# Optimization experiments

Hardware: AMD Instinct MI355X
Metric: run time of the kernel (lower is better)

Reference implementation:

```python
import jax, jax.numpy as jnp
import numpy as np
import math

B, T, H = 16, 4096, 768
D = 64      # attention_head_size
M = 256     # number of random features


def setup_inputs() -> dict:
    key = jax.random.key(0)
    ks = jax.random.split(key, 8)
    s = 1.0 / math.sqrt(H)
    x = jax.random.normal(ks[0], (B, T, H), dtype=jnp.float32)
    Wq = jax.random.uniform(ks[1], (H, D), jnp.float32, -s, s)
    bq = jax.random.uniform(ks[2], (D,), jnp.float32, -s, s)
    Wk = jax.random.uniform(ks[3], (H, D), jnp.float32, -s, s)
    bk = jax.random.uniform(ks[4], (D,), jnp.float32, -s, s)
    Wv = jax.random.uniform(ks[5], (H, D), jnp.float32, -s, s)
    bv = jax.random.uniform(ks[6], (D,), jnp.float32, -s, s)
    w = jax.random.normal(ks[7], (M, D), dtype=jnp.float32)  # frozen random features
    return {"x": x, "Wq": Wq, "bq": bq, "Wk": Wk, "bk": bk, "Wv": Wv, "bv": bv, "w": w}


def _prm_exp(z, w):
    # z: [B,T,D], w: [M,D] -> [B,T,M]
    xd = 0.5 * jnp.sum(z * z, axis=-1, keepdims=True)          # [B,T,1]
    wtx = jnp.einsum('bti,mi->btm', z, w)                      # [B,T,M]
    return jnp.exp(wtx - xd) / math.sqrt(w.shape[0])


def reference(x, Wq, bq, Wk, bk, Wv, bv, w):
    q = x @ Wq + bq                                            # [B,T,D]
    k = x @ Wk + bk
    v = x @ Wv + bv
    qp = _prm_exp(q, w)                                        # [B,T,M]
    kp = _prm_exp(k, w)                                        # [B,T,M]
    Dn = jnp.einsum('bti,bi->bt', qp, kp.sum(axis=1))[:, :, None]   # [B,T,1]
    kptv = jnp.einsum('bin,bim->bnm', v, kp)                   # [B,D,M]
    attn_out = jnp.einsum('bti,bni->btn', qp, kptv) / Dn       # [B,T,D]
    return attn_out, kptv
```

## Files before the change

kernel.cpp:

```cpp
#include <hip/hip_runtime.h>
#include <math.h>

#define BB 16
#define TT 4096
#define HH 768
#define DD 64
#define MM 256
#define BT (BB*TT)
#define TSPLIT 16

__device__ __forceinline__ void fma4(float& acc, float4 a, float4 b){
    acc = __builtin_fmaf(a.x, b.x, acc);
    acc = __builtin_fmaf(a.y, b.y, acc);
    acc = __builtin_fmaf(a.z, b.z, acc);
    acc = __builtin_fmaf(a.w, b.w, acc);
}

__global__ __launch_bounds__(256) void qkv_kernel(
    const float* __restrict__ x,
    const float* __restrict__ Wq, const float* __restrict__ bq,
    const float* __restrict__ Wk, const float* __restrict__ bk,
    const float* __restrict__ Wv, const float* __restrict__ bv,
    float* __restrict__ q, float* __restrict__ k, float* __restrict__ v)
{
    __shared__ float xs[64][36];
    __shared__ float ws[32][196];
    const int tid = threadIdx.x;
    const int row0 = blockIdx.x * 64;
    const int tr = tid >> 4, tc = tid & 15;

    float4 acc[4][3];
    #pragma unroll
    for (int r = 0; r < 4; r++)
        #pragma unroll
        for (int c = 0; c < 3; c++) acc[r][c] = make_float4(0.f,0.f,0.f,0.f);

    for (int kc = 0; kc < HH; kc += 32){
        __syncthreads();
        #pragma unroll
        for (int i = 0; i < 2; i++){
            int l = tid + i*256;
            int r = l >> 3, j4 = (l & 7) << 2;
            *(float4*)&xs[r][j4] = *(const float4*)&x[(size_t)(row0+r)*HH + kc + j4];
        }
        #pragma unroll
        for (int i = 0; i < 2; i++){
            int l = tid + i*256;
            int kk = l >> 4, c4 = (l & 15) << 2;
            *(float4*)&ws[kk][c4]       = *(const float4*)&Wq[(size_t)(kc+kk)*DD + c4];
            *(float4*)&ws[kk][64 + c4]  = *(const float4*)&Wk[(size_t)(kc+kk)*DD + c4];
            *(float4*)&ws[kk][128 + c4] = *(const float4*)&Wv[(size_t)(kc+kk)*DD + c4];
        }
        __syncthreads();
        #pragma unroll
        for (int kk = 0; kk < 32; kk++){
            float xv[4];
            float4 wv[3];
            #pragma unroll
            for (int r = 0; r < 4; r++) xv[r] = xs[tr*4+r][kk];
            #pragma unroll
            for (int c = 0; c < 3; c++) wv[c] = *(float4*)&ws[kk][tc*12 + c*4];
            #pragma unroll
            for (int r = 0; r < 4; r++)
                #pragma unroll
                for (int c = 0; c < 3; c++){
                    acc[r][c].x = __builtin_fmaf(xv[r], wv[c].x, acc[r][c].x);
                    acc[r][c].y = __builtin_fmaf(xv[r], wv[c].y, acc[r][c].y);
                    acc[r][c].z = __builtin_fmaf(xv[r], wv[c].z, acc[r][c].z);
                    acc[r][c].w = __builtin_fmaf(xv[r], wv[c].w, acc[r][c].w);
                }
        }
    }
    #pragma unroll
    for (int c = 0; c < 3; c++){
        int col = tc*12 + c*4;
        int sel = col >> 6;
        int d = col & 63;
        const float* bias = (sel==0) ? bq : (sel==1) ? bk : bv;
        float* dst = (sel==0) ? q : (sel==1) ? k : v;
        float4 b4 = *(const float4*)&bias[d];
        #pragma unroll
        for (int r = 0; r < 4; r++){
            size_t grow = (size_t)(row0 + tr*4 + r);
            float4 o;
            o.x = acc[r][c].x + b4.x;
            o.y = acc[r][c].y + b4.y;
            o.z = acc[r][c].z + b4.z;
            o.w = acc[r][c].w + b4.w;
            *(float4*)&dst[grow*DD + d] = o;
        }
    }
}

__global__ __launch_bounds__(256) void kp_kernel(
    const float* __restrict__ k, const float* __restrict__ w,
    float* __restrict__ kp, float* __restrict__ ksum)
{
    __shared__ float ks_[64][68];
    __shared__ float ws_[64][68];
    __shared__ float xd_s[64];
    __shared__ float ksum_s[256];
    const int tid = threadIdx.x;
    const int row0 = blockIdx.x * 64;
    const int b = row0 >> 12;
    const int tr = tid >> 4, tc = tid & 15;

    #pragma unroll
    for (int i = 0; i < 4; i++){
        int l = tid + i*256;
        int r = l >> 4, c4 = (l & 15) << 2;
        *(float4*)&ks_[r][c4] = *(const float4*)&k[(size_t)(row0+r)*DD + c4];
    }
    ksum_s[tid] = 0.f;
    __syncthreads();
    {
        int rowx = tid >> 2, sub = tid & 3;
        float s = 0.f;
        #pragma unroll
        for (int j = 0; j < 4; j++){
            float4 kv = *(float4*)&ks_[rowx][sub*16 + j*4];
            s += kv.x*kv.x + kv.y*kv.y + kv.z*kv.z + kv.w*kv.w;
        }
        s += __shfl_xor(s, 1);
        s += __shfl_xor(s, 2);
        if (sub == 0) xd_s[rowx] = 0.5f * s;
    }

    for (int mc = 0; mc < 4; mc++){
        __syncthreads();
        #pragma unroll
        for (int i = 0; i < 4; i++){
            int l = tid + i*256;
            int r = l >> 4, c4 = (l & 15) << 2;
            *(float4*)&ws_[r][c4] = *(const float4*)&w[(size_t)(mc*64 + r)*DD + c4];
        }
        __syncthreads();
        float acc[4][4];
        #pragma unroll
        for (int r = 0; r < 4; r++)
            #pragma unroll
            for (int c = 0; c < 4; c++) acc[r][c] = 0.f;
        #pragma unroll
        for (int d4 = 0; d4 < 16; d4++){
            float4 qv[4], wv[4];
            #pragma unroll
            for (int r = 0; r < 4; r++) qv[r] = *(float4*)&ks_[tr*4+r][d4*4];
            #pragma unroll
            for (int c = 0; c < 4; c++) wv[c] = *(float4*)&ws_[tc + 16*c][d4*4];
            #pragma unroll
            for (int r = 0; r < 4; r++)
                #pragma unroll
                for (int c = 0; c < 4; c++) fma4(acc[r][c], qv[r], wv[c]);
        }
        float colsum[4] = {0.f, 0.f, 0.f, 0.f};
        #pragma unroll
        for (int r = 0; r < 4; r++){
            float xd = xd_s[tr*4+r];
            #pragma unroll
            for (int c = 0; c < 4; c++){
                float val = expf(acc[r][c] - xd) * 0.0625f;
                colsum[c] += val;
                kp[(size_t)(row0 + tr*4 + r)*MM + mc*64 + tc + 16*c] = val;
            }
        }
        #pragma unroll
        for (int c = 0; c < 4; c++)
            atomicAdd(&ksum_s[mc*64 + tc + 16*c], colsum[c]);
    }
    __syncthreads();
    unsafeAtomicAdd(&ksum[b*MM + tid], ksum_s[tid]);
}

__global__ __launch_bounds__(256) void kptv_kernel(
    const float* __restrict__ v, const float* __restrict__ kp,
    float* __restrict__ out_kptv)
{
    __shared__ float vs[32][68];
    __shared__ float kps[32][68];
    const int tid = threadIdx.x;
    const int b  = blockIdx.z;
    const int mc = blockIdx.y;
    const int t0 = blockIdx.x * (TT/TSPLIT);
    const int tn = tid >> 4, tm = tid & 15;

    float acc[4][4];
    #pragma unroll
    for (int r = 0; r < 4; r++)
        #pragma unroll
        for (int c = 0; c < 4; c++) acc[r][c] = 0.f;

    for (int tt = 0; tt < TT/TSPLIT; tt += 32){
        __syncthreads();
        #pragma unroll
        for (int i = 0; i < 2; i++){
            int l = tid + i*256;
            int r = l >> 4, c4 = (l & 15) << 2;
            *(float4*)&vs[r][c4]  = *(const float4*)&v [(size_t)(b*TT + t0 + tt + r)*DD + c4];
            *(float4*)&kps[r][c4] = *(const float4*)&kp[(size_t)(b*TT + t0 + tt + r)*MM + mc*64 + c4];
        }
        __syncthreads();
        #pragma unroll
        for (int t = 0; t < 32; t++){
            float vv[4], kv[4];
            *(float4*)vv = *(float4*)&vs[t][tn*4];
            *(float4*)kv = *(float4*)&kps[t][tm*4];
            #pragma unroll
            for (int r = 0; r < 4; r++)
                #pragma unroll
                for (int c = 0; c < 4; c++)
                    acc[r][c] = __builtin_fmaf(vv[r], kv[c], acc[r][c]);
        }
    }
    #pragma unroll
    for (int r = 0; r < 4; r++)
        #pragma unroll
        for (int c = 0; c < 4; c++)
            unsafeAtomicAdd(&out_kptv[(size_t)b*DD*MM + (size_t)(tn*4+r)*MM + mc*64 + tm*4 + c],
                            acc[r][c]);
}

__global__ __launch_bounds__(256) void attn_kernel(
    const float* __restrict__ q, const float* __restrict__ w,
    const float* __restrict__ kptv, const float* __restrict__ ksum,
    float* __restrict__ out)
{
    __shared__ float qs[64][68];
    __shared__ float wqp[64][68];
    __shared__ float kvs[64][68];
    __shared__ float ksum_s[256];
    __shared__ float xd_s[64];
    const int tid = threadIdx.x;
    const int row0 = blockIdx.x * 64;
    const int b = row0 >> 12;
    const int tr = tid >> 4, tc = tid & 15;

    #pragma unroll
    for (int i = 0; i < 4; i++){
        int l = tid + i*256;
        int r = l >> 4, c4 = (l & 15) << 2;
        *(float4*)&qs[r][c4] = *(const float4*)&q[(size_t)(row0 + r)*DD + c4];
    }
    ksum_s[tid] = ksum[b*MM + tid];
    __syncthreads();
    {
        int rowx = tid >> 2, sub = tid & 3;
        float s = 0.f;
        #pragma unroll
        for (int j = 0; j < 4; j++){
            float4 qv = *(float4*)&qs[rowx][sub*16 + j*4];
            s += qv.x*qv.x + qv.y*qv.y + qv.z*qv.z + qv.w*qv.w;
        }
        s += __shfl_xor(s, 1);
        s += __shfl_xor(s, 2);
        if (sub == 0) xd_s[rowx] = 0.5f * s;
    }

    float acc2[4][4];
    float dn[4];
    #pragma unroll
    for (int r = 0; r < 4; r++){
        dn[r] = 0.f;
        #pragma unroll
        for (int c = 0; c < 4; c++) acc2[r][c] = 0.f;
    }

    for (int mc = 0; mc < 4; mc++){
        __syncthreads();
        #pragma unroll
        for (int i = 0; i < 4; i++){
            int l = tid + i*256;
            int r = l >> 4, c4 = (l & 15) << 2;
            *(float4*)&wqp[r][c4] = *(const float4*)&w[(size_t)(mc*64 + r)*DD + c4];
            *(float4*)&kvs[r][c4] = *(const float4*)&kptv[(size_t)b*DD*MM + r*MM + mc*64 + c4];
        }
        __syncthreads();
        float acc1[4][4];
        #pragma unroll
        for (int r = 0; r < 4; r++)
            #pragma unroll
            for (int c = 0; c < 4; c++) acc1[r][c] = 0.f;
        #pragma unroll
        for (int d4 = 0; d4 < 16; d4++){
            float4 qv[4], wv[4];
            #pragma unroll
            for (int r = 0; r < 4; r++) qv[r] = *(float4*)&qs[tr*4+r][d4*4];
            #pragma unroll
            for (int c = 0; c < 4; c++) wv[c] = *(float4*)&wqp[tc + 16*c][d4*4];
            #pragma unroll
            for (int r = 0; r < 4; r++)
                #pragma unroll
                for (int c = 0; c < 4; c++) fma4(acc1[r][c], qv[r], wv[c]);
        }
        float qp_[4][4];
        #pragma unroll
        for (int r = 0; r < 4; r++){
            float xd = xd_s[tr*4+r];
            #pragma unroll
            for (int c = 0; c < 4; c++){
                float val = expf(acc1[r][c] - xd) * 0.0625f;
                qp_[r][c] = val;
                dn[r] = __builtin_fmaf(val, ksum_s[mc*64 + tc + 16*c], dn[r]);
            }
        }
        __syncthreads();
        #pragma unroll
        for (int r = 0; r < 4; r++)
            #pragma unroll
            for (int c = 0; c < 4; c++)
                wqp[tr*4+r][tc + 16*c] = qp_[r][c];
        __syncthreads();
        #pragma unroll
        for (int m4 = 0; m4 < 16; m4++){
            float4 qv[4], kv[4];
            #pragma unroll
            for (int r = 0; r < 4; r++) qv[r] = *(float4*)&wqp[tr*4+r][m4*4];
            #pragma unroll
            for (int c = 0; c < 4; c++) kv[c] = *(float4*)&kvs[tc + 16*c][m4*4];
            #pragma unroll
            for (int r = 0; r < 4; r++)
                #pragma unroll
                for (int c = 0; c < 4; c++) fma4(acc2[r][c], qv[r], kv[c]);
        }
    }
    #pragma unroll
    for (int r = 0; r < 4; r++){
        dn[r] += __shfl_xor(dn[r], 1);
        dn[r] += __shfl_xor(dn[r], 2);
        dn[r] += __shfl_xor(dn[r], 4);
        dn[r] += __shfl_xor(dn[r], 8);
    }
    #pragma unroll
    for (int r = 0; r < 4; r++){
        float inv = 1.0f / dn[r];
        #pragma unroll
        for (int c = 0; c < 4; c++)
            out[(size_t)(row0 + tr*4 + r)*DD + tc + 16*c] = acc2[r][c] * inv;
    }
}

extern "C" void kernel_launch(void* const* d_in, const int* in_sizes, int n_in,
                              void* d_out, int out_size, void* d_ws, size_t ws_size,
                              hipStream_t stream) {
    const float* x  = (const float*)d_in[0];
    const float* Wq = (const float*)d_in[1];
    const float* bq = (const float*)d_in[2];
    const float* Wk = (const float*)d_in[3];
    const float* bk = (const float*)d_in[4];
    const float* Wv = (const float*)d_in[5];
    const float* bv = (const float*)d_in[6];
    const float* w  = (const float*)d_in[7];

    float* out_attn = (float*)d_out;
    float* out_kptv = out_attn + (size_t)BB*TT*DD;

    float* q    = (float*)d_ws;
    float* k    = q + (size_t)BT*DD;
    float* v    = k + (size_t)BT*DD;
    float* kp   = v + (size_t)BT*DD;
    float* ksum = kp + (size_t)BT*MM;

    hipMemsetAsync(out_kptv, 0, (size_t)BB*DD*MM*sizeof(float), stream);
    hipMemsetAsync(ksum, 0, (size_t)BB*MM*sizeof(float), stream);

    qkv_kernel<<<BT/64, 256, 0, stream>>>(x, Wq, bq, Wk, bk, Wv, bv, q, k, v);
    kp_kernel<<<BT/64, 256, 0, stream>>>(k, w, kp, ksum);
    kptv_kernel<<<dim3(TSPLIT, 4, BB), 256, 0, stream>>>(v, kp, out_kptv);
    attn_kernel<<<BT/64, 256, 0, stream>>>(q, w, out_kptv, ksum, out_attn);
}
```

Measured before the change: 679.9 us.

## Move QKV projection to bf16x3 split-precision MFMA with pre-converted weights

Replaces the FP32 SIMT QKV GEMM with a matrix-core kernel that splits each operand into bf16 hi and lo parts and accumulates three MFMA products, keeping near-FP32 accuracy. A small pre-pass converts the weights into a transposed, K-blocked hi/lo bf16 layout and packs the biases. The x tile is split to hi/lo on the fly while loading into shared memory. The goal is to cut the FP32 FMA cost of the largest GEMM. In exchange it adds conversion ALU work, an extra launch, and scalar, less-coalesced output stores.

```diff
diff --git a/kernel.cpp b/kernel.cpp
--- a/kernel.cpp
+++ b/kernel.cpp
@@ -9,6 +9,23 @@
 #define BT (BB*TT)
 #define TSPLIT 16
 
+typedef __attribute__((ext_vector_type(8))) short bf16x8;
+typedef __attribute__((ext_vector_type(4))) float f32x4;
+
+union frag_u { bf16x8 v; ushort4 h[2]; };
+
+__device__ __forceinline__ bf16x8 ld_frag(const unsigned short* p){
+    frag_u u;
+    u.h[0] = *(const ushort4*)p;
+    u.h[1] = *(const ushort4*)(p + 4);
+    return u.v;
+}
+__device__ __forceinline__ void st8(unsigned short* p, bf16x8 t){
+    frag_u u; u.v = t;
+    *(ushort4*)p       = u.h[0];
+    *(ushort4*)(p + 4) = u.h[1];
+}
+
 __device__ __forceinline__ void fma4(float& acc, float4 a, float4 b){
     acc = __builtin_fmaf(a.x, b.x, acc);
     acc = __builtin_fmaf(a.y, b.y, acc);
@@ -16,78 +33,125 @@
     acc = __builtin_fmaf(a.w, b.w, acc);
 }
 
-__global__ __launch_bounds__(256) void qkv_kernel(
+__device__ __forceinline__ unsigned short f2bf_rn(float f){
+    unsigned u = __builtin_bit_cast(unsigned, f);
+    unsigned r = u + 0x7FFFu + ((u >> 16) & 1u);
+    return (unsigned short)(r >> 16);
+}
+__device__ __forceinline__ float bf2f(unsigned short h){
+    unsigned u = ((unsigned)h) << 16;
+    return __builtin_bit_cast(float, u);
+}
+
+__global__ __launch_bounds__(256) void wcvt_kernel(
+    const float* __restrict__ Wq, const float* __restrict__ Wk, const float* __restrict__ Wv,
+    const float* __restrict__ bq, const float* __restrict__ bk, const float* __restrict__ bv,
+    unsigned short* __restrict__ wt_hi, unsigned short* __restrict__ wt_lo,
+    float* __restrict__ bias_all)
+{
+    int idx = blockIdx.x * 256 + threadIdx.x;
+    int n = idx / 768, kk = idx - n*768;
+    int sel = n >> 6, d = n & 63;
+    const float* W = (sel==0) ? Wq : (sel==1) ? Wk : Wv;
+    float f = W[kk*DD + d];
+    unsigned short hi = f2bf_rn(f);
+    float lo = f - bf2f(hi);
+    unsigned short lov = f2bf_rn(lo);
+    size_t off = ((size_t)(kk >> 5)*192 + n)*32 + (kk & 31);
+    wt_hi[off] = hi;
+    wt_lo[off] = lov;
+    if (idx < 192)
+        bias_all[idx] = (idx < 64) ? bq[idx] : (idx < 128) ? bk[idx-64] : bv[idx-128];
+}
+
+__global__ __launch_bounds__(512) void qkv_mfma_kernel(
     const float* __restrict__ x,
-    const float* __restrict__ Wq, const float* __restrict__ bq,
-    const float* __restrict__ Wk, const float* __restrict__ bk,
-    const float* __restrict__ Wv, const float* __restrict__ bv,
+    const unsigned short* __restrict__ wt_hi, const unsigned short* __restrict__ wt_lo,
+    const float* __restrict__ bias_all,
     float* __restrict__ q, float* __restrict__ k, float* __restrict__ v)
 {
-    __shared__ float xs[64][36];
-    __shared__ float ws[32][196];
-    const int tid = threadIdx.x;
-    const int row0 = blockIdx.x * 64;
-    const int tr = tid >> 4, tc = tid & 15;
-
-    float4 acc[4][3];
-    #pragma unroll
-    for (int r = 0; r < 4; r++)
-        #pragma unroll
-        for (int c = 0; c < 3; c++) acc[r][c] = make_float4(0.f,0.f,0.f,0.f);
+    __shared__ unsigned short Ah[128][40];
+    __shared__ unsigned short Al[128][40];
+    __shared__ unsigned short Bh[192][40];
+    __shared__ unsigned short Bl[192][40];
+    const int tid  = threadIdx.x;
+    const int lane = tid & 63;
+    const int wid  = tid >> 6;
+    const int wm   = wid & 3;
+    const int wn   = wid >> 2;
+    const int row0 = blockIdx.x * 128;
+
+    f32x4 acc[2][6] = {};
 
     for (int kc = 0; kc < HH; kc += 32){
         __syncthreads();
         #pragma unroll
         for (int i = 0; i < 2; i++){
-            int l = tid + i*256;
-            int r = l >> 3, j4 = (l & 7) << 2;
-            *(float4*)&xs[r][j4] = *(const float4*)&x[(size_t)(row0+r)*HH + kc + j4];
-        }
-        #pragma unroll
-        for (int i = 0; i < 2; i++){
-            int l = tid + i*256;
-            int kk = l >> 4, c4 = (l & 15) << 2;
-            *(float4*)&ws[kk][c4]       = *(const float4*)&Wq[(size_t)(kc+kk)*DD + c4];
-            *(float4*)&ws[kk][64 + c4]  = *(const float4*)&Wk[(size_t)(kc+kk)*DD + c4];
-            *(float4*)&ws[kk][128 + c4] = *(const float4*)&Wv[(size_t)(kc+kk)*DD + c4];
-        }
-        __syncthreads();
-        #pragma unroll
-        for (int kk = 0; kk < 32; kk++){
-            float xv[4];
-            float4 wv[3];
-            #pragma unroll
-            for (int r = 0; r < 4; r++) xv[r] = xs[tr*4+r][kk];
-            #pragma unroll
-            for (int c = 0; c < 3; c++) wv[c] = *(float4*)&ws[kk][tc*12 + c*4];
-            #pragma unroll
-            for (int r = 0; r < 4; r++)
-                #pragma unroll
-                for (int c = 0; c < 3; c++){
-                    acc[r][c].x = __builtin_fmaf(xv[r], wv[c].x, acc[r][c].x);
-                    acc[r][c].y = __builtin_fmaf(xv[r], wv[c].y, acc[r][c].y);
-                    acc[r][c].z = __builtin_fmaf(xv[r], wv[c].z, acc[r][c].z);
-                    acc[r][c].w = __builtin_fmaf(xv[r], wv[c].w, acc[r][c].w);
+            int l = tid + i*512;
+            int r = l >> 3, c4 = (l & 7) << 2;
+            float4 xv = *(const float4*)&x[(size_t)(row0 + r)*HH + kc + c4];
+            ushort4 hv, lv;
+            hv.x = f2bf_rn(xv.x); lv.x = f2bf_rn(xv.x - bf2f(hv.x));
+            hv.y = f2bf_rn(xv.y); lv.y = f2bf_rn(xv.y - bf2f(hv.y));
+            hv.z = f2bf_rn(xv.z); lv.z = f2bf_rn(xv.z - bf2f(hv.z));
+            hv.w = f2bf_rn(xv.w); lv.w = f2bf_rn(xv.w - bf2f(hv.w));
+            *(ushort4*)&Ah[r][c4] = hv;
+            *(ushort4*)&Al[r][c4] = lv;
+        }
+        {
+            const unsigned short* srch = wt_hi + (size_t)(kc >> 5)*192*32;
+            const unsigned short* srcl = wt_lo + (size_t)(kc >> 5)*192*32;
+            #pragma unroll
+            for (int i = 0; i < 3; i++){
+                int l = tid + i*512;
+                if (l < 768){
+                    int r = l >> 2, c8 = (l & 3) << 3;
+                    bf16x8 t = *(const bf16x8*)(srch + (size_t)l*8);
+                    st8(&Bh[r][c8], t);
+                } else {
+                    int l2 = l - 768;
+                    int r = l2 >> 2, c8 = (l2 & 3) << 3;
+                    bf16x8 t = *(const bf16x8*)(srcl + (size_t)l2*8);
+                    st8(&Bl[r][c8], t);
                 }
-        }
-    }
-    #pragma unroll
-    for (int c = 0; c < 3; c++){
-        int col = tc*12 + c*4;
-        int sel = col >> 6;
-        int d = col & 63;
-        const float* bias = (sel==0) ? bq : (sel==1) ? bk : bv;
+            }
+        }
+        __syncthreads();
+        bf16x8 ah[2], al[2];
+        #pragma unroll
+        for (int mi = 0; mi < 2; mi++){
+            int ar = wm*32 + mi*16 + (lane & 15);
+            int ak = (lane >> 4) << 3;
+            ah[mi] = ld_frag(&Ah[ar][ak]);
+            al[mi] = ld_frag(&Al[ar][ak]);
+        }
+        #pragma unroll
+        for (int ni = 0; ni < 6; ni++){
+            int bc = wn*96 + ni*16 + (lane & 15);
+            int bk_ = (lane >> 4) << 3;
+            bf16x8 bh = ld_frag(&Bh[bc][bk_]);
+            bf16x8 bl = ld_frag(&Bl[bc][bk_]);
+            #pragma unroll
+            for (int mi = 0; mi < 2; mi++){
+                acc[mi][ni] = __builtin_amdgcn_mfma_f32_16x16x32_bf16(ah[mi], bh, acc[mi][ni], 0, 0, 0);
+                acc[mi][ni] = __builtin_amdgcn_mfma_f32_16x16x32_bf16(ah[mi], bl, acc[mi][ni], 0, 0, 0);
+                acc[mi][ni] = __builtin_amdgcn_mfma_f32_16x16x32_bf16(al[mi], bh, acc[mi][ni], 0, 0, 0);
+            }
+        }
+    }
+    #pragma unroll
+    for (int ni = 0; ni < 6; ni++){
+        int col = wn*96 + ni*16 + (lane & 15);
+        int sel = col >> 6, d = col & 63;
+        float bias = bias_all[col];
         float* dst = (sel==0) ? q : (sel==1) ? k : v;
-        float4 b4 = *(const float4*)&bias[d];
-        #pragma unroll
-        for (int r = 0; r < 4; r++){
-            size_t grow = (size_t)(row0 + tr*4 + r);
-            float4 o;
-            o.x = acc[r][c].x + b4.x;
-            o.y = acc[r][c].y + b4.y;
-            o.z = acc[r][c].z + b4.z;
-            o.w = acc[r][c].w + b4.w;
-            *(float4*)&dst[grow*DD + d] = o;
+        #pragma unroll
+        for (int mi = 0; mi < 2; mi++){
+            int rbase = row0 + wm*32 + mi*16 + ((lane >> 4) << 2);
+            #pragma unroll
+            for (int j = 0; j < 4; j++){
+                dst[(size_t)(rbase + j)*DD + d] = acc[mi][ni][j] + bias;
+            }
         }
     }
 }
@@ -358,11 +422,15 @@
     float* v    = k + (size_t)BT*DD;
     float* kp   = v + (size_t)BT*DD;
     float* ksum = kp + (size_t)BT*MM;
+    unsigned short* wt_hi = (unsigned short*)(ksum + BB*MM);
+    unsigned short* wt_lo = wt_hi + (size_t)HH*192;
+    float* bias_all = (float*)(wt_lo + (size_t)HH*192);
 
     hipMemsetAsync(out_kptv, 0, (size_t)BB*DD*MM*sizeof(float), stream);
     hipMemsetAsync(ksum, 0, (size_t)BB*MM*sizeof(float), stream);
 
-    qkv_kernel<<<BT/64, 256, 0, stream>>>(x, Wq, bq, Wk, bk, Wv, bv, q, k, v);
+    wcvt_kernel<<<(HH*192)/256, 256, 0, stream>>>(Wq, Wk, Wv, bq, bk, bv, wt_hi, wt_lo, bias_all);
+    qkv_mfma_kernel<<<BT/128, 512, 0, stream>>>(x, wt_hi, wt_lo, bias_all, q, k, v);
     kp_kernel<<<BT/64, 256, 0, stream>>>(k, w, kp, ksum);
     kptv_kernel<<<dim3(TSPLIT, 4, BB), 256, 0, stream>>>(v, kp, out_kptv);
     attn_kernel<<<BT/64, 256, 0, stream>>>(q, w, out_kptv, ksum, out_attn);
```

New measurement: 546.2 us. 1.24x faster.
